# Kernel tuning notes

Hardware: AMD Instinct MI355X
Metric: run time of the kernel (lower is better)

The kernel has to match this reference:

```python
import jax, jax.numpy as jnp
import numpy as np

SR = 22050
L = 2097153            # output_size = int(SR*95.109); equals NFFT//2+1 so spectral broadcast is well-defined
NFFT = 4194304         # 2**ceil(log2(L))
BANDS = [(1.0, 4.0), (4.0, 8.0), (8.0, 13.0), (13.0, 30.0), (30.0, 100.0), (100.0, 200.0)]
SPEC = [7.83, 528.0, 396.0, 2.5, 14.1, 432.0, 6.0, 30.0]
WIN = 15               # min(15, NFFT//100)
FREQS_NP = np.fft.rfftfreq(NFFT, 1.0 / SR).astype(np.float32)
FREQS = jnp.asarray(FREQS_NP)


def _freq_mod(sig, band_w, freq_w, harm_prog, tm_w1, tm_b1, tm_w2, tm_b2, tm_w3, tm_b3):
    t = jnp.arange(L, dtype=jnp.float32)
    Xf = jnp.fft.rfft(jnp.pad(sig, (0, NFFT - L)))            # [L] complex64
    # sequential band enhancements == product of per-band multipliers
    mult = jnp.ones((L,), jnp.float32)
    for b, (lo, hi) in enumerate(BANDS):
        c = (lo + hi) / 2.0
        w = (hi - lo) / 2.0
        mask = jnp.exp(-0.5 * ((FREQS - c) / (w / 2.0)) ** 2)
        mask = jnp.where((FREQS < lo) | (FREQS > hi), 0.0, mask)
        tmod = jnp.sin(2.0 * np.pi * c * t / SR)
        mult = mult * (1.0 + mask * band_w[b] * (1.0 + 0.2 * tmod))
    # harmonic progression (identical for every specific frequency -> compute once)
    tn = (t / L)[:, None]
    h = jax.nn.relu(tn @ tm_w1 + tm_b1)
    h = jax.nn.relu(h @ tm_w2 + tm_b2)
    mp = h @ tm_w3 + tm_b3                                    # [L, 8]
    chord_idx = jnp.floor(t / L * 8.0).astype(jnp.int32) % 8
    chord = harm_prog[chord_idx] * (1.0 + mp[:, 1] * jnp.sin(2.0 * np.pi * t / L))[:, None]
    prog_mean = chord.mean()
    # specific-frequency harmonic windows (static indices; commutative multiplies)
    smult = jnp.ones((L,), jnp.float32)
    for k, f in enumerate(SPEC):
        for m in (1.0, 2.0, 3.0, 4.0, 5.0):
            hf = f * m
            if hf >= SR / 2:
                continue
            hidx = int(np.argmin(np.abs(FREQS_NP - hf)))
            s = max(0, hidx - WIN)
            e = min(L - 1, hidx + WIN)
            win = jnp.asarray(np.exp(-0.5 * ((np.arange(s, e + 1) - hidx) / (WIN / 3.0)) ** 2).astype(np.float32))
            enh = freq_w[k] * win * (1.0 / m ** 1.2) * (1.0 + prog_mean)
            smult = smult.at[s:e + 1].multiply(1.0 + enh)
    Xf = Xf * mult * smult
    mag = jnp.abs(Xf)
    ph = jnp.angle(Xf)
    mag_s = jnp.concatenate([mag[:1], mag[1:-1] * 0.7 + mag[:-2] * 0.15 + mag[2:] * 0.15, mag[-1:]])
    Xc = mag_s * jnp.exp(1j * ph)
    return jnp.fft.irfft(Xc, n=NFFT)[:L]


def _conv1d(x, w, b, stride):
    y = jax.lax.conv_general_dilated(x, w, (stride,), [(2, 2)], dimension_numbers=("NCH", "OIH", "NCH"))
    return y + b[None, :, None]


def setup_inputs() -> dict:
    key = jax.random.key(0)
    ks = jax.random.split(key, 16)
    n = lambda k, s, sc=1.0: jax.random.normal(k, s, dtype=jnp.float32) * sc
    return {
        "z": n(ks[0], (1, 1, L)),
        "condition": n(ks[1], (1, 8)),
        "band_w": jnp.full((6,), 0.5, jnp.float32),
        "freq_w": jnp.full((8,), 0.3, jnp.float32),
        "harm_prog": n(ks[2], (8, 4)),
        "tm_w1": n(ks[3], (1, 32), 0.5), "tm_b1": jnp.zeros((32,), jnp.float32),
        "tm_w2": n(ks[4], (32, 16), 0.2), "tm_b2": jnp.zeros((16,), jnp.float32),
        "tm_w3": n(ks[5], (16, 8), 0.2), "tm_b3": jnp.zeros((8,), jnp.float32),
        "c1_w": n(ks[6], (32, 1, 5), 0.3), "c1_b": jnp.zeros((32,), jnp.float32),
        "c2_w": n(ks[7], (64, 32, 5), 0.08), "c2_b": jnp.zeros((64,), jnp.float32),
        "c3_w": n(ks[8], (128, 64, 5), 0.05), "c3_b": jnp.zeros((128,), jnp.float32),
        "mx_w1": n(ks[9], (192, 256), 0.07), "mx_b1": jnp.zeros((256,), jnp.float32),
        "mx_w2": n(ks[10], (256, 1), 0.06), "mx_b2": jnp.zeros((1,), jnp.float32),
    }


def reference(z, condition, band_w, freq_w, harm_prog, tm_w1, tm_b1, tm_w2, tm_b2, tm_w3, tm_b3,
              c1_w, c1_b, c2_w, c2_b, c3_w, c3_b, mx_w1, mx_b1, mx_w2, mx_b2):
    base = _freq_mod(z[0, 0], band_w, freq_w, harm_prog, tm_w1, tm_b1, tm_w2, tm_b2, tm_w3, tm_b3)[None, None, :]
    h = jax.nn.leaky_relu(_conv1d(base, c1_w, c1_b, 2), 0.2)
    h = jax.nn.leaky_relu(_conv1d(h, c2_w, c2_b, 2), 0.2)
    h = jax.nn.leaky_relu(_conv1d(h, c3_w, c3_b, 2), 0.2)
    feat = h.mean(axis=2)                                     # [1, 128]
    emb = jnp.zeros((1, 64), jnp.float32)                     # instrument_idx=None path
    mixed = jnp.concatenate([feat, emb], axis=1)              # [1, 192]
    out = jax.nn.leaky_relu(mixed @ mx_w1 + mx_b1, 0.2) @ mx_w2 + mx_b2
    return out
```

## Files before the change

### kernel.cpp

```cpp
#include <hip/hip_runtime.h>
#include <cmath>

#define LSIG  2097153
#define MH    2097152
#define NFFTC 4194304
#define NT128 16384
#define O1C   1048577
#define O2C   524289
#define O3C   262145

#define TO3   62
#define NB3   4229

#define A_OFF    0
#define B_OFF    16777216
#define PM_OFF   58720268
#define FEAT_OFF 58720272
#define W2Q_OFF  50331664
#define W3Q_OFF  50352144
#define W1Q_OFF  50434064

struct SmultTab { int hidx[40]; float inv12[40]; int fk[40]; int maxe; };

typedef short short8 __attribute__((ext_vector_type(8)));
typedef float f32x4v __attribute__((ext_vector_type(4)));

union AFrag { uint4 q; short8 s; };
union BFrag { uint4 q; unsigned int u[4]; short8 s; };

__device__ __forceinline__ float lrelu(float a){ return a > 0.0f ? a : 0.2f*a; }

__device__ __forceinline__ float hsin(float rev){ return __builtin_amdgcn_sinf(rev); }
__device__ __forceinline__ float hcos(float rev){ return __builtin_amdgcn_cosf(rev); }

__device__ __forceinline__ unsigned int rbf(float f) {
  unsigned int u = __float_as_uint(f);
  u += 0x7fffu + ((u >> 16) & 1u);
  return u >> 16;
}
__device__ __forceinline__ unsigned int pack_bf2(float a, float b) {
  unsigned int r;
  asm("v_cvt_pk_bf16_f32 %0, %1, %2" : "=v"(r) : "v"(a), "v"(b));
  return r;
}

__device__ __forceinline__ int swz1(int pos, int dw) {
  return (pos*16 + dw) ^ (((pos >> 1) & 7) << 2);
}
__device__ __forceinline__ int swz2(int pos, int dw) {
  return (pos*32 + dw) ^ (((pos >> 1) & 7) << 2);
}

__device__ __forceinline__ int slot128(int jj, int q) {
  int s = q ^ ((q >> 4) & 7);
  return jj*128 + ((s + 9*jj) & 127);
}

__device__ __forceinline__ float2 cadd(float2 a, float2 b){ return make_float2(a.x+b.x, a.y+b.y); }
__device__ __forceinline__ float2 csub(float2 a, float2 b){ return make_float2(a.x-b.x, a.y-b.y); }

template<bool FWD> __device__ __forceinline__ float2 jrot(float2 z){
  return FWD ? make_float2(z.y, -z.x) : make_float2(-z.y, z.x);
}

template<bool FWD> __device__ __forceinline__ void dft8(float2 v[8]) {
  const float cq = 0.70710678118654752440f;
  const float S  = FWD ? -1.0f : 1.0f;
  float2 e0 = cadd(v[0], v[4]), e1 = csub(v[0], v[4]);
  float2 e2 = cadd(v[2], v[6]), e3 = csub(v[2], v[6]);
  float2 E0 = cadd(e0, e2), E2 = csub(e0, e2);
  float2 jt = jrot<FWD>(e3);
  float2 E1 = cadd(e1, jt), E3 = csub(e1, jt);
  float2 o0 = cadd(v[1], v[5]), o1 = csub(v[1], v[5]);
  float2 o2 = cadd(v[3], v[7]), o3 = csub(v[3], v[7]);
  float2 O0 = cadd(o0, o2), O2 = csub(o0, o2);
  float2 jo = jrot<FWD>(o3);
  float2 O1 = cadd(o1, jo), O3 = csub(o1, jo);
  float2 w1 = make_float2(cq*O1.x - S*cq*O1.y, cq*O1.y + S*cq*O1.x);
  float2 w2 = jrot<FWD>(O2);
  float2 w3 = make_float2(-cq*O3.x - S*cq*O3.y, -cq*O3.y + S*cq*O3.x);
  v[0] = cadd(E0, O0); v[4] = csub(E0, O0);
  v[1] = cadd(E1, w1); v[5] = csub(E1, w1);
  v[2] = cadd(E2, w2); v[6] = csub(E2, w2);
  v[3] = cadd(E3, w3); v[7] = csub(E3, w3);
}

template<bool FWD>
__device__ __forceinline__ void fft128_body(float2* stage, int t, int jb, int Ns) {
  const float ssg = FWD ? -1.0f : 1.0f;
  const float invden = 1.0f / (float)(128 * Ns);
  {
    const int jj = t >> 4, b = t & 15;
    const int m = (jb + jj) & (Ns - 1);
    float2 v[8];
#pragma unroll
    for (int a = 0; a < 8; ++a) {
      const int r = 16*a + b;
      float2 x = stage[slot128(jj, r)];
      if (Ns > 1) {
        float rev = (float)(m * r) * invden;
        float sn = ssg * hsin(rev), cs = hcos(rev);
        x = make_float2(x.x*cs - x.y*sn, x.x*sn + x.y*cs);
      }
      v[a] = x;
    }
    dft8<FWD>(v);
#pragma unroll
    for (int d = 0; d < 8; ++d)
      stage[slot128(jj, 16*d + b)] = v[d];
  }
  __syncthreads();
  {
    float2 y[16];
    const int jj = (t & 255) >> 3, d = t & 7;
    if (t < 256) {
#pragma unroll
      for (int b = 0; b < 16; ++b) {
        float2 x = stage[slot128(jj, 16*d + b)];
        float rev = (float)(b*d) * 0.0078125f;
        float sn = ssg * hsin(rev), cs = hcos(rev);
        y[b] = make_float2(x.x*cs - x.y*sn, x.x*sn + x.y*cs);
      }
    }
    __syncthreads();
    if (t < 256) {
      float2 E[8], O[8];
#pragma unroll
      for (int b = 0; b < 8; ++b) { E[b] = y[2*b]; O[b] = y[2*b+1]; }
      dft8<FWD>(E);
      dft8<FWD>(O);
#pragma unroll
      for (int c = 0; c < 8; ++c) {
        float rev = (float)c * 0.0625f;
        float sn = ssg * hsin(rev), cs = hcos(rev);
        float2 To = make_float2(O[c].x*cs - O[c].y*sn, O[c].x*sn + O[c].y*cs);
        stage[slot128(jj, 8*c + d)]      = cadd(E[c], To);
        stage[slot128(jj, 8*c + 64 + d)] = csub(E[c], To);
      }
    }
  }
  __syncthreads();
}

template<bool FWD, bool TRUNC>
__global__ __launch_bounds__(512) void kfft128(const float2* __restrict__ src,
                                               float2* __restrict__ dst, int Ns) {
  __shared__ float2 stage[4096];
  const int t = threadIdx.x;
  const int jb = blockIdx.x * 32;
  for (int c = 0; c < 4; ++c) {
    int u = t + 512*c;
    int jp = u & 15, rr = u >> 4;
    float4 q = *(const float4*)&src[jb + 2*jp + rr*NT128];
    stage[slot128(2*jp,   rr)] = make_float2(q.x, q.y);
    stage[slot128(2*jp+1, rr)] = make_float2(q.z, q.w);
  }
  __syncthreads();
  fft128_body<FWD>(stage, t, jb, Ns);
  if (Ns == 1) {
    for (int c = 0; c < 4; ++c) {
      int u = t + 512*c;
      int jj = u >> 6, k2 = (u & 63) * 2;
      float2 a = stage[slot128(jj, k2)], b = stage[slot128(jj, k2+1)];
      *(float4*)&dst[(jb + jj)*128 + k2] = make_float4(a.x, a.y, b.x, b.y);
    }
  } else {
    for (int c = 0; c < 4; ++c) {
      int u = t + 512*c;
      int pi = u & 15, k = u >> 4;
      int jj = 2*pi, j2 = jb + jj, m2 = j2 & (Ns - 1);
      int base = (j2 - m2)*128 + m2 + k*Ns;
      if (TRUNC && k >= 64) {
        if (k == 64 && j2 == 0) dst[base] = stage[slot128(jj, k)];
        continue;
      }
      float2 a = stage[slot128(jj, k)], b = stage[slot128(jj+1, k)];
      *(float4*)&dst[base] = make_float4(a.x, a.y, b.x, b.y);
    }
  }
}

__global__ __launch_bounds__(512) void kfirst(
    const float* __restrict__ zin, float2* __restrict__ dst,
    const float* __restrict__ tw1, const float* __restrict__ tb1,
    const float* __restrict__ tw2, const float* __restrict__ tb2,
    const float* __restrict__ tw3, const float* __restrict__ tb3,
    const float* __restrict__ hp, float* __restrict__ pm,
    float* __restrict__ feat) {
  __shared__ float2 stage[4096];
  __shared__ float shp[8];
  __shared__ float red[512];
  const int t = threadIdx.x;
  const int bb = blockIdx.x;
  if (bb < 512) {
    const int jb = bb * 32;
    for (int c = 0; c < 4; ++c) {
      int u = t + 512*c;
      int jp = u & 15, rr = u >> 4;
      int n = jb + 2*jp + rr*NT128;
      float2 a0, a1;
      if (n < 1048576) {
        float4 q = *(const float4*)&((const float2*)zin)[n];
        a0 = make_float2(q.x, q.y); a1 = make_float2(q.z, q.w);
      } else if (n == 1048576) {
        a0 = make_float2(zin[2097152], 0.0f); a1 = make_float2(0.0f, 0.0f);
      } else {
        a0 = make_float2(0.0f, 0.0f); a1 = a0;
      }
      stage[slot128(2*jp,   rr)] = a0;
      stage[slot128(2*jp+1, rr)] = a1;
    }
    __syncthreads();
    fft128_body<true>(stage, t, jb, 1);
    for (int c = 0; c < 4; ++c) {
      int u = t + 512*c;
      int jj = u >> 6, k2 = (u & 63) * 2;
      float2 a = stage[slot128(jj, k2)], b = stage[slot128(jj, k2+1)];
      *(float4*)&dst[(jb + jj)*128 + k2] = make_float4(a.x, a.y, b.x, b.y);
    }
    return;
  }
  if (t < 8) { float s = 0.f; for (int j = 0; j < 4; ++j) s += hp[t*4+j]; shp[t] = s; }
  __syncthreads();
  const int gid = (bb - 512)*512 + t;
  if (gid < 32768) feat[gid] = 0.0f;
  const float Lf = 2097153.0f;
  float tnv[4], sv[4];
  int ci[4];
  float acc[4][16];
#pragma unroll
  for (int e = 0; e < 4; ++e) {
    float ti = (float)(gid + e*524288);
    float tn = ti / Lf;
    tnv[e] = tn;
    sv[e] = hsin(tn);
    ci[e] = ((int)floorf(tn * 8.0f)) & 7;
#pragma unroll
    for (int kk = 0; kk < 16; ++kk) acc[e][kk] = tb2[kk];
  }
  for (int j = 0; j < 32; ++j) {
    float a = tw1[j], b = tb1[j];
    float hj[4];
#pragma unroll
    for (int e = 0; e < 4; ++e) hj[e] = fmaxf(a*tnv[e] + b, 0.0f);
#pragma unroll
    for (int kk = 0; kk < 16; ++kk) {
      float w = tw2[j*16 + kk];
#pragma unroll
      for (int e = 0; e < 4; ++e) acc[e][kk] += hj[e]*w;
    }
  }
  float lsum = 0.0f;
  const float b31 = tb3[1];
#pragma unroll
  for (int e = 0; e < 4; ++e) {
    float mp1 = b31;
#pragma unroll
    for (int kk = 0; kk < 16; ++kk) mp1 += fmaxf(acc[e][kk], 0.0f)*tw3[kk*8+1];
    lsum += shp[ci[e]] * (1.0f + mp1*sv[e]);
  }
  if (gid == 0) {
    float ti = 2097152.0f;
    float tn = ti / Lf;
    float a1[16];
    for (int kk = 0; kk < 16; ++kk) a1[kk] = tb2[kk];
    for (int j = 0; j < 32; ++j) {
      float h = fmaxf(tw1[j]*tn + tb1[j], 0.0f);
      for (int kk = 0; kk < 16; ++kk) a1[kk] += h*tw2[j*16+kk];
    }
    float mp1 = b31;
    for (int kk = 0; kk < 16; ++kk) mp1 += fmaxf(a1[kk], 0.0f)*tw3[kk*8+1];
    float svx = hsin(tn);
    int cix = ((int)floorf(tn * 8.0f)) & 7;
    lsum += shp[cix] * (1.0f + mp1*svx);
  }
  red[t] = lsum;
  __syncthreads();
  for (int off = 256; off > 0; off >>= 1) {
    if (t < off) red[t] += red[t+off];
    __syncthreads();
  }
  if (t == 0) atomicAdd(pm, red[0]);
}

__device__ __forceinline__ float2 xsplit(float2 zk, float2 zm, float rev) {
  float2 s  = make_float2(zk.x + zm.x, zk.y - zm.y);
  float2 dd = make_float2(zk.x - zm.x, zk.y + zm.y);
  float sn = -hsin(rev), cs = hcos(rev);
  float2 t1 = make_float2(cs*dd.x - sn*dd.y, cs*dd.y + sn*dd.x);
  return make_float2(0.5f*(s.x + t1.y), 0.5f*(s.y - t1.x));
}
__device__ __forceinline__ float2 scale_xc(float2 c, float mg, float ms) {
  if (mg > 0.0f) { float sc = ms/mg; return make_float2(c.x*sc, c.y*sc); }
  return make_float2(ms, 0.0f);
}
__device__ __forceinline__ float2 invpack(int n, float2 a, float2 b) {
  float2 s  = make_float2(a.x + b.x, a.y - b.y);
  float2 dd = make_float2(a.x - b.x, a.y + b.y);
  float rev = (float)n * (1.0f / (float)NFFTC);
  float sn = hsin(rev), cs = hcos(rev);
  float2 xo = make_float2(0.5f*(cs*dd.x - sn*dd.y), 0.5f*(cs*dd.y + sn*dd.x));
  const float sc = 1.0f / (float)MH;
  return make_float2((0.5f*s.x - xo.y)*sc, (0.5f*s.y + xo.x)*sc);
}

__global__ __launch_bounds__(256) void kspectral(const float2* __restrict__ Z,
    float2* __restrict__ A, const float* __restrict__ bwp,
    const float* __restrict__ fwp, const float* __restrict__ pm_in, SmultTab tab,
    const float* __restrict__ c1w, const float* __restrict__ c2w,
    const float* __restrict__ c3w, unsigned short* __restrict__ w1q,
    unsigned short* __restrict__ w2q, unsigned short* __restrict__ w3q) {
  const int bb = blockIdx.x;
  const int t = threadIdx.x;
  if (bb >= 4096) {
    int i = (bb - 4096)*256 + t;
    if (i < 1024) {
      int e = i & 7, u4 = i >> 3;
      int col = u4 & 15, quad = (u4 >> 4) & 3, mi = u4 >> 6;
      float v = (quad == 0 && e < 5) ? c1w[(mi*16 + col)*5 + e] : 0.0f;
      w1q[i] = (unsigned short)rbf(v);
    }
    if (i < 10240) {
      int e = i & 7, u4 = i >> 3;
      int col = u4 & 15, quad = (u4 >> 4) & 3, mtkt = u4 >> 6;
      int kt = mtkt % 5, mt = mtkt / 5;
      int ch = mt*16 + col, c1 = quad*8 + e;
      w2q[i] = (unsigned short)rbf(c2w[ch*160 + c1*5 + kt]);
    }
    if (i < 40960) {
      int e = i & 7, u4 = i >> 3;
      int col = u4 & 15, quad = (u4 >> 4) & 3, mtkt = u4 >> 6;
      int kt = mtkt % 10, mt = mtkt / 10;
      int ch = mt*16 + col, c2 = (kt & 1)*32 + quad*8 + e;
      w3q[i] = (unsigned short)rbf(c3w[ch*320 + c2*5 + (kt >> 1)]);
    }
    return;
  }
  __shared__ float2 Xlo[258], Xhi[258];
  __shared__ float  Mlo[258], Mhi[258];
  const int k0 = bb * 256;
  const float pm1 = 1.0f + pm_in[0] * (1.0f/8388612.0f);
  for (int w = t; w < 258; w += 256) {
    int k = k0 - 1 + w;
    float2 zk = Z[k & (MH-1)];
    float2 zm = Z[(MH - k) & (MH-1)];
    {
      float2 X = xsplit(zk, zm, (float)k * (1.0f/(float)NFFTC));
      float mv = 1.0f;
      if (k <= 38050) {
        const float blo[6] = {1.0f,4.0f,8.0f,13.0f,30.0f,100.0f};
        const float bhi[6] = {4.0f,8.0f,13.0f,30.0f,100.0f,200.0f};
        const float bcn[6] = {2.5f,6.0f,10.5f,21.5f,65.0f,150.0f};
        const float bhw[6] = {0.75f,1.0f,1.25f,4.25f,17.5f,25.0f};
        float f = (float)((double)k * (22050.0/4194304.0));
#pragma unroll
        for (int b = 0; b < 6; ++b) {
          if (f >= blo[b] && f <= bhi[b]) {
            float q = (f - bcn[b]) / bhw[b];
            float mask = expf(-0.5f*q*q);
            double frd = (double)k * ((double)bcn[b] / 22050.0);
            frd -= floor(frd);
            float tm = hsin((float)frd);
            mv *= (1.0f + mask * bwp[b] * (1.0f + 0.2f*tm));
          }
        }
      }
      if (k <= tab.maxe) {
        for (int ww = 0; ww < 40; ++ww) {
          int dlt = k - tab.hidx[ww];
          if (dlt >= -15 && dlt <= 15) {
            float x = (float)dlt * 0.2f;
            float win = expf(-0.5f*x*x);
            float enh = fwp[tab.fk[ww]] * win * tab.inv12[ww] * pm1;
            mv *= (1.0f + enh);
          }
        }
      }
      X.x *= mv; X.y *= mv;
      Xlo[w] = X; Mlo[w] = sqrtf(X.x*X.x + X.y*X.y);
    }
    {
      float2 X = xsplit(zm, zk, (float)(MH - k) * (1.0f/(float)NFFTC));
      Xhi[w] = X; Mhi[w] = sqrtf(X.x*X.x + X.y*X.y);
    }
  }
  __syncthreads();
  const int k = k0 + t, w = t + 1;
  float msl = (k == 0) ? Mlo[w] : 0.7f*Mlo[w] + 0.15f*(Mlo[w-1] + Mlo[w+1]);
  float2 xl = scale_xc(Xlo[w], Mlo[w], msl);
  float msh = (k == 0) ? Mhi[w] : 0.7f*Mhi[w] + 0.15f*(Mhi[w+1] + Mhi[w-1]);
  float2 xh = scale_xc(Xhi[w], Mhi[w], msh);
  A[k] = invpack(k, xl, xh);
  if (k >= 1) A[MH - k] = invpack(MH - k, xh, xl);
  if (bb == 4095 && t == 255) {
    float2 Xm = Xlo[257]; float Mm = Mlo[257];
    float ms = 0.7f*Mm + 0.15f*(Mlo[256] + Mhi[256]);
    float2 xm = scale_xc(Xm, Mm, ms);
    A[1048576] = invpack(1048576, xm, xm);
  }
}

__global__ __launch_bounds__(256, 4) void kconv(const float* __restrict__ x,
    const unsigned short* __restrict__ w1q, const unsigned short* __restrict__ w2q,
    const unsigned short* __restrict__ w3q, const float* __restrict__ c1b,
    const float* __restrict__ c2b, const float* __restrict__ c3b,
    float* __restrict__ feat) {
  __shared__ float sb[552];
  __shared__ unsigned int sh1[4352];
  __shared__ unsigned int sh2[4224];
  const int tid  = threadIdx.x;
  const int blk  = blockIdx.x;
  const int s3   = blk * TO3;
  const int lane = tid & 63;
  const int wv   = tid >> 6;
  const int col  = lane & 15;
  const int quad = lane >> 4;

  const uint4* W1 = (const uint4*)w1q;
  AFrag a1w[2];
#pragma unroll
  for (int mi = 0; mi < 2; ++mi)
    a1w[mi].q = W1[(mi*4 + quad)*16 + col];

  const uint4* W2 = (const uint4*)w2q;
  const int mt2 = (wv & 1) * 2;
  const int ntb2 = (wv >> 1) * 4;
  uint4 wk2[2][5];
#pragma unroll
  for (int mi = 0; mi < 2; ++mi)
#pragma unroll
    for (int kt = 0; kt < 5; ++kt)
      wk2[mi][kt] = W2[(((mt2+mi)*5 + kt)*4 + quad)*16 + col];

  float b1r[2][4], b2r[2][4];
#pragma unroll
  for (int mi = 0; mi < 2; ++mi)
#pragma unroll
    for (int r = 0; r < 4; ++r) {
      b1r[mi][r] = c1b[mi*16 + quad*4 + r];
      b2r[mi][r] = c2b[(mt2+mi)*16 + quad*4 + r];
    }

  {
    const int pb = 8*s3 - 14;
    for (int idx = tid; idx < 552; idx += 256) {
      int p = pb + idx;
      sb[idx] = (idx < 517 && p >= 0 && p < LSIG) ? x[p] : 0.0f;
    }
    if (tid < 128) sh2[4096 + tid] = 0u;
  }
  __syncthreads();

  {
    const int a1 = 4*s3 - 6;
    for (int nt = wv; nt < 17; nt += 4) {
      const int n = nt*16 + col;
      BFrag bf;
      if (quad == 0) {
        const float* ps = &sb[2*n];
        bf.u[0] = pack_bf2(ps[0], ps[1]);
        bf.u[1] = pack_bf2(ps[2], ps[3]);
        bf.u[2] = pack_bf2(ps[4], ps[5]);
        bf.u[3] = pack_bf2(ps[6], ps[7]);
      } else {
        bf.u[0] = 0u; bf.u[1] = 0u; bf.u[2] = 0u; bf.u[3] = 0u;
      }
      f32x4v acc[2];
      acc[0] = (f32x4v){b1r[0][0], b1r[0][1], b1r[0][2], b1r[0][3]};
      acc[1] = (f32x4v){b1r[1][0], b1r[1][1], b1r[1][2], b1r[1][3]};
      acc[0] = __builtin_amdgcn_mfma_f32_16x16x32_bf16(a1w[0].s, bf.s, acc[0], 0, 0, 0);
      acc[1] = __builtin_amdgcn_mfma_f32_16x16x32_bf16(a1w[1].s, bf.s, acc[1], 0, 0, 0);
      const int o1 = a1 + n;
      const bool ok = (n <= 257) && (o1 >= 0) && (o1 < O1C);
#pragma unroll
      for (int mi = 0; mi < 2; ++mi) {
        float v0 = ok ? lrelu(acc[mi][0]) : 0.0f;
        float v1 = ok ? lrelu(acc[mi][1]) : 0.0f;
        float v2 = ok ? lrelu(acc[mi][2]) : 0.0f;
        float v3 = ok ? lrelu(acc[mi][3]) : 0.0f;
        uint2 pk; pk.x = pack_bf2(v0, v1); pk.y = pack_bf2(v2, v3);
        *(uint2*)&sh1[swz1(n, mi*8 + quad*2)] = pk;
      }
    }
  }
  __syncthreads();

  f32x4v acc2[2][4];
#pragma unroll
  for (int mi = 0; mi < 2; ++mi)
#pragma unroll
    for (int nt = 0; nt < 4; ++nt)
      acc2[mi][nt] = (f32x4v){b2r[mi][0], b2r[mi][1], b2r[mi][2], b2r[mi][3]};
#pragma unroll
  for (int kt = 0; kt < 5; ++kt) {
#pragma unroll
    for (int nt = 0; nt < 4; ++nt) {
      const int n = (ntb2 + nt)*16 + col;
      const int row = 2*n + kt;
      BFrag bf;
      bf.q = *(const uint4*)&sh1[swz1(row, quad*4)];
      AFrag a0, a1; a0.q = wk2[0][kt]; a1.q = wk2[1][kt];
      acc2[0][nt] = __builtin_amdgcn_mfma_f32_16x16x32_bf16(a0.s, bf.s, acc2[0][nt], 0, 0, 0);
      acc2[1][nt] = __builtin_amdgcn_mfma_f32_16x16x32_bf16(a1.s, bf.s, acc2[1][nt], 0, 0, 0);
    }
  }

  {
    const int a2 = 2*s3 - 2;
#pragma unroll
    for (int nt = 0; nt < 4; ++nt) {
      const int p = (ntb2 + nt)*16 + col;
      const int o2 = a2 + p;
      const bool ok = (o2 >= 0) && (o2 < O2C);
#pragma unroll
      for (int mi = 0; mi < 2; ++mi) {
        float v0 = ok ? lrelu(acc2[mi][nt][0]) : 0.0f;
        float v1 = ok ? lrelu(acc2[mi][nt][1]) : 0.0f;
        float v2 = ok ? lrelu(acc2[mi][nt][2]) : 0.0f;
        float v3 = ok ? lrelu(acc2[mi][nt][3]) : 0.0f;
        const int dwb = (mt2+mi)*8 + quad*2;
        uint2 pk; pk.x = pack_bf2(v0, v1); pk.y = pack_bf2(v2, v3);
        *(uint2*)&sh2[swz2(p, dwb)] = pk;
      }
    }
  }
  __syncthreads();

  {
    const uint4* W3 = (const uint4*)w3q;
    const int slot = (blk & 255) * 128;
#pragma unroll
    for (int pass = 0; pass < 2; ++pass) {
      const int mt = wv + 4*pass;
      uint4 wk3[10];
#pragma unroll
      for (int kt = 0; kt < 10; ++kt)
        wk3[kt] = W3[((mt*10 + kt)*4 + quad)*16 + col];
      float b3r[4];
#pragma unroll
      for (int r = 0; r < 4; ++r) b3r[r] = c3b[mt*16 + quad*4 + r];
      f32x4v acc3[4];
#pragma unroll
      for (int nt = 0; nt < 4; ++nt)
        acc3[nt] = (f32x4v){b3r[0], b3r[1], b3r[2], b3r[3]};
#pragma unroll
      for (int kt = 0; kt < 10; ++kt) {
        const int tap = kt >> 1;
        const int hh  = (kt & 1) * 16;
#pragma unroll
        for (int nt = 0; nt < 4; ++nt) {
          const int n = nt*16 + col;
          const int row = 2*n + tap;
          BFrag bf;
          bf.q = *(const uint4*)&sh2[swz2(row, hh + quad*4)];
          AFrag a; a.q = wk3[kt];
          acc3[nt] = __builtin_amdgcn_mfma_f32_16x16x32_bf16(a.s, bf.s, acc3[nt], 0, 0, 0);
        }
      }
#pragma unroll
      for (int r = 0; r < 4; ++r) {
        const int ch = mt*16 + quad*4 + r;
        float v = 0.0f;
#pragma unroll
        for (int nt = 0; nt < 4; ++nt) {
          const int n = nt*16 + col;
          const bool ok = (n < TO3) && (s3 + n < O3C);
          if (ok) v += lrelu(acc3[nt][r]);
        }
        v += __shfl_xor(v, 1);
        v += __shfl_xor(v, 2);
        v += __shfl_xor(v, 4);
        v += __shfl_xor(v, 8);
        if (col == 0) atomicAdd(&feat[slot + ch], v);
      }
    }
  }
}

__global__ __launch_bounds__(256) void kfinal(const float* __restrict__ feat,
    const float* __restrict__ mw1, const float* __restrict__ mb1,
    const float* __restrict__ mw2, const float* __restrict__ mb2,
    float* __restrict__ out) {
  __shared__ float sfeat[128];
  __shared__ float red[256];
  const int tid = threadIdx.x;
  if (tid < 128) {
    float s = 0.0f;
    for (int sl = 0; sl < 256; ++sl) s += feat[sl*128 + tid];
    sfeat[tid] = s / 262145.0f;
  }
  __syncthreads();
  float y = mb1[tid];
  for (int i = 0; i < 128; ++i) y += sfeat[i] * mw1[i*256 + tid];
  y = y > 0.0f ? y : 0.2f*y;
  red[tid] = y * mw2[tid];
  __syncthreads();
  for (int off = 128; off > 0; off >>= 1) {
    if (tid < off) red[tid] += red[tid+off];
    __syncthreads();
  }
  if (tid == 0) out[0] = red[0] + mb2[0];
}

extern "C" void kernel_launch(void* const* d_in, const int* in_sizes, int n_in,
                              void* d_out, int out_size, void* d_ws, size_t ws_size,
                              hipStream_t stream) {
  (void)in_sizes; (void)n_in; (void)out_size; (void)ws_size;
  const float* z   = (const float*)d_in[0];
  const float* bw  = (const float*)d_in[2];
  const float* fw  = (const float*)d_in[3];
  const float* hp  = (const float*)d_in[4];
  const float* tw1 = (const float*)d_in[5];
  const float* tb1 = (const float*)d_in[6];
  const float* tw2 = (const float*)d_in[7];
  const float* tb2 = (const float*)d_in[8];
  const float* tw3 = (const float*)d_in[9];
  const float* tb3 = (const float*)d_in[10];
  const float* c1w = (const float*)d_in[11];
  const float* c1b = (const float*)d_in[12];
  const float* c2w = (const float*)d_in[13];
  const float* c2b = (const float*)d_in[14];
  const float* c3w = (const float*)d_in[15];
  const float* c3b = (const float*)d_in[16];
  const float* mw1 = (const float*)d_in[17];
  const float* mb1 = (const float*)d_in[18];
  const float* mw2 = (const float*)d_in[19];
  const float* mb2 = (const float*)d_in[20];

  char* wsb = (char*)d_ws;
  float2* A    = (float2*)(wsb + A_OFF);
  float2* B    = (float2*)(wsb + B_OFF);
  float*  PM   = (float*)(wsb + PM_OFF);
  float*  FEAT = (float*)(wsb + FEAT_OFF);
  unsigned short* W1Q = (unsigned short*)(wsb + W1Q_OFF);
  unsigned short* W2Q = (unsigned short*)(wsb + W2Q_OFF);
  unsigned short* W3Q = (unsigned short*)(wsb + W3Q_OFF);

  SmultTab tab;
  {
    const double spec[8] = {7.83, 528.0, 396.0, 2.5, 14.1, 432.0, 6.0, 30.0};
    int n = 0, maxe = 0;
    for (int kk = 0; kk < 8; ++kk)
      for (int m = 1; m <= 5; ++m) {
        double hf = spec[kk] * (double)m;
        if (hf >= 11025.0) continue;
        int hidx = (int)std::floor(hf * (4194304.0/22050.0) + 0.5);
        tab.hidx[n]  = hidx;
        tab.inv12[n] = (float)(1.0/std::pow((double)m, 1.2));
        tab.fk[n]    = kk;
        if (hidx + 15 > maxe) maxe = hidx + 15;
        ++n;
      }
    tab.maxe = maxe;
  }

  (void)hipMemsetAsync(wsb + PM_OFF, 0, 4, stream);

  kfirst<<<1536,512,0,stream>>>(z, A, tw1,tb1,tw2,tb2,tw3,tb3,hp, PM, FEAT);

  kfft128<true,false><<<512,512,0,stream>>>(A, B, 128);
  kfft128<true,false><<<512,512,0,stream>>>(B, A, 16384);

  kspectral<<<4256,256,0,stream>>>(A, B, bw, fw, PM, tab, c1w, c2w, c3w, W1Q, W2Q, W3Q);

  kfft128<false,false><<<512,512,0,stream>>>(B, A, 1);
  kfft128<false,false><<<512,512,0,stream>>>(A, B, 128);
  kfft128<false,true ><<<512,512,0,stream>>>(B, A, 16384);

  kconv<<<NB3,256,0,stream>>>((const float*)A, W1Q, W2Q, W3Q, c1b, c2b, c3b, FEAT);
  kfinal<<<1,256,0,stream>>>(FEAT, mw1, mb1, mw2, mb2, (float*)d_out);
}
```

Before: 254.7 us.

## Double conv tile per block and use all FFT threads in final radix-16 stage

```diff
diff --git a/kernel.cpp b/kernel.cpp
--- a/kernel.cpp
+++ b/kernel.cpp
@@ -9,8 +9,8 @@
 #define O2C   524289
 #define O3C   262145
 
-#define TO3   62
-#define NB3   4229
+#define TO3   124
+#define NB3   2115
 
 #define A_OFF    0
 #define B_OFF    16777216
@@ -111,32 +111,33 @@
   }
   __syncthreads();
   {
-    float2 y[16];
-    const int jj = (t & 255) >> 3, d = t & 7;
-    if (t < 256) {
-#pragma unroll
-      for (int b = 0; b < 16; ++b) {
-        float2 x = stage[slot128(jj, 16*d + b)];
-        float rev = (float)(b*d) * 0.0078125f;
-        float sn = ssg * hsin(rev), cs = hcos(rev);
-        y[b] = make_float2(x.x*cs - x.y*sn, x.x*sn + x.y*cs);
-      }
-    }
-    __syncthreads();
-    if (t < 256) {
-      float2 E[8], O[8];
-#pragma unroll
-      for (int b = 0; b < 8; ++b) { E[b] = y[2*b]; O[b] = y[2*b+1]; }
-      dft8<FWD>(E);
-      dft8<FWD>(O);
+    const int jj = t >> 4, d = (t >> 1) & 7, par = t & 1;
+    float2 h[8];
+#pragma unroll
+    for (int bp = 0; bp < 8; ++bp) {
+      const int b = 2*bp + par;
+      float2 x = stage[slot128(jj, 16*d + b)];
+      float rev = (float)(b*d) * 0.0078125f;
+      float sn = ssg * hsin(rev), cs = hcos(rev);
+      h[bp] = make_float2(x.x*cs - x.y*sn, x.x*sn + x.y*cs);
+    }
+    dft8<FWD>(h);
+    if (par) {
 #pragma unroll
       for (int c = 0; c < 8; ++c) {
         float rev = (float)c * 0.0625f;
         float sn = ssg * hsin(rev), cs = hcos(rev);
-        float2 To = make_float2(O[c].x*cs - O[c].y*sn, O[c].x*sn + O[c].y*cs);
-        stage[slot128(jj, 8*c + d)]      = cadd(E[c], To);
-        stage[slot128(jj, 8*c + 64 + d)] = csub(E[c], To);
-      }
+        h[c] = make_float2(h[c].x*cs - h[c].y*sn, h[c].x*sn + h[c].y*cs);
+      }
+    }
+    __syncthreads();
+    const float sgn = par ? -1.0f : 1.0f;
+    const int off = d + (par << 6);
+#pragma unroll
+    for (int c = 0; c < 8; ++c) {
+      float px = __shfl_xor(h[c].x, 1);
+      float py = __shfl_xor(h[c].y, 1);
+      stage[slot128(jj, 8*c + off)] = make_float2(px + sgn*h[c].x, py + sgn*h[c].y);
     }
   }
   __syncthreads();
@@ -400,14 +401,14 @@
   }
 }
 
-__global__ __launch_bounds__(256, 4) void kconv(const float* __restrict__ x,
+__global__ __launch_bounds__(512, 4) void kconv(const float* __restrict__ x,
     const unsigned short* __restrict__ w1q, const unsigned short* __restrict__ w2q,
     const unsigned short* __restrict__ w3q, const float* __restrict__ c1b,
     const float* __restrict__ c2b, const float* __restrict__ c3b,
     float* __restrict__ feat) {
-  __shared__ float sb[552];
-  __shared__ unsigned int sh1[4352];
-  __shared__ unsigned int sh2[4224];
+  __shared__ float sb[1064];
+  __shared__ unsigned int sh1[8448];
+  __shared__ unsigned int sh2[8448];
   const int tid  = threadIdx.x;
   const int blk  = blockIdx.x;
   const int s3   = blk * TO3;
@@ -443,17 +444,17 @@
 
   {
     const int pb = 8*s3 - 14;
-    for (int idx = tid; idx < 552; idx += 256) {
+    for (int idx = tid; idx < 1064; idx += 512) {
       int p = pb + idx;
-      sb[idx] = (idx < 517 && p >= 0 && p < LSIG) ? x[p] : 0.0f;
-    }
-    if (tid < 128) sh2[4096 + tid] = 0u;
+      sb[idx] = (idx < 1005 && p >= 0 && p < LSIG) ? x[p] : 0.0f;
+    }
+    if (tid < 256) sh2[8192 + tid] = 0u;
   }
   __syncthreads();
 
   {
     const int a1 = 4*s3 - 6;
-    for (int nt = wv; nt < 17; nt += 4) {
+    for (int nt = wv; nt < 33; nt += 8) {
       const int n = nt*16 + col;
       BFrag bf;
       if (quad == 0) {
@@ -471,7 +472,7 @@
       acc[0] = __builtin_amdgcn_mfma_f32_16x16x32_bf16(a1w[0].s, bf.s, acc[0], 0, 0, 0);
       acc[1] = __builtin_amdgcn_mfma_f32_16x16x32_bf16(a1w[1].s, bf.s, acc[1], 0, 0, 0);
       const int o1 = a1 + n;
-      const bool ok = (n <= 257) && (o1 >= 0) && (o1 < O1C);
+      const bool ok = (n <= 507) && (o1 >= 0) && (o1 < O1C);
 #pragma unroll
       for (int mi = 0; mi < 2; ++mi) {
         float v0 = ok ? lrelu(acc[mi][0]) : 0.0f;
@@ -529,50 +530,47 @@
   {
     const uint4* W3 = (const uint4*)w3q;
     const int slot = (blk & 255) * 128;
-#pragma unroll
-    for (int pass = 0; pass < 2; ++pass) {
-      const int mt = wv + 4*pass;
-      uint4 wk3[10];
-#pragma unroll
-      for (int kt = 0; kt < 10; ++kt)
-        wk3[kt] = W3[((mt*10 + kt)*4 + quad)*16 + col];
-      float b3r[4];
-#pragma unroll
-      for (int r = 0; r < 4; ++r) b3r[r] = c3b[mt*16 + quad*4 + r];
-      f32x4v acc3[4];
-#pragma unroll
-      for (int nt = 0; nt < 4; ++nt)
-        acc3[nt] = (f32x4v){b3r[0], b3r[1], b3r[2], b3r[3]};
-#pragma unroll
-      for (int kt = 0; kt < 10; ++kt) {
-        const int tap = kt >> 1;
-        const int hh  = (kt & 1) * 16;
-#pragma unroll
-        for (int nt = 0; nt < 4; ++nt) {
-          const int n = nt*16 + col;
-          const int row = 2*n + tap;
-          BFrag bf;
-          bf.q = *(const uint4*)&sh2[swz2(row, hh + quad*4)];
-          AFrag a; a.q = wk3[kt];
-          acc3[nt] = __builtin_amdgcn_mfma_f32_16x16x32_bf16(a.s, bf.s, acc3[nt], 0, 0, 0);
-        }
-      }
-#pragma unroll
-      for (int r = 0; r < 4; ++r) {
-        const int ch = mt*16 + quad*4 + r;
-        float v = 0.0f;
-#pragma unroll
-        for (int nt = 0; nt < 4; ++nt) {
-          const int n = nt*16 + col;
-          const bool ok = (n < TO3) && (s3 + n < O3C);
-          if (ok) v += lrelu(acc3[nt][r]);
-        }
-        v += __shfl_xor(v, 1);
-        v += __shfl_xor(v, 2);
-        v += __shfl_xor(v, 4);
-        v += __shfl_xor(v, 8);
-        if (col == 0) atomicAdd(&feat[slot + ch], v);
-      }
+    const int mt = wv;
+    uint4 wk3[10];
+#pragma unroll
+    for (int kt = 0; kt < 10; ++kt)
+      wk3[kt] = W3[((mt*10 + kt)*4 + quad)*16 + col];
+    float b3r[4];
+#pragma unroll
+    for (int r = 0; r < 4; ++r) b3r[r] = c3b[mt*16 + quad*4 + r];
+    f32x4v acc3[8];
+#pragma unroll
+    for (int nt = 0; nt < 8; ++nt)
+      acc3[nt] = (f32x4v){b3r[0], b3r[1], b3r[2], b3r[3]};
+#pragma unroll
+    for (int kt = 0; kt < 10; ++kt) {
+      const int tap = kt >> 1;
+      const int hh  = (kt & 1) * 16;
+#pragma unroll
+      for (int nt = 0; nt < 8; ++nt) {
+        const int n = nt*16 + col;
+        const int row = 2*n + tap;
+        BFrag bf;
+        bf.q = *(const uint4*)&sh2[swz2(row, hh + quad*4)];
+        AFrag a; a.q = wk3[kt];
+        acc3[nt] = __builtin_amdgcn_mfma_f32_16x16x32_bf16(a.s, bf.s, acc3[nt], 0, 0, 0);
+      }
+    }
+#pragma unroll
+    for (int r = 0; r < 4; ++r) {
+      const int ch = mt*16 + quad*4 + r;
+      float v = 0.0f;
+#pragma unroll
+      for (int nt = 0; nt < 8; ++nt) {
+        const int n = nt*16 + col;
+        const bool ok = (n < TO3) && (s3 + n < O3C);
+        if (ok) v += lrelu(acc3[nt][r]);
+      }
+      v += __shfl_xor(v, 1);
+      v += __shfl_xor(v, 2);
+      v += __shfl_xor(v, 4);
+      v += __shfl_xor(v, 8);
+      if (col == 0) atomicAdd(&feat[slot + ch], v);
     }
   }
 }
@@ -667,6 +665,6 @@
   kfft128<false,false><<<512,512,0,stream>>>(A, B, 128);
   kfft128<false,true ><<<512,512,0,stream>>>(B, A, 16384);
 
-  kconv<<<NB3,256,0,stream>>>((const float*)A, W1Q, W2Q, W3Q, c1b, c2b, c3b, FEAT);
+  kconv<<<NB3,512,0,stream>>>((const float*)A, W1Q, W2Q, W3Q, c1b, c2b, c3b, FEAT);
   kfinal<<<1,256,0,stream>>>(FEAT, mw1, mb1, mw2, mb2, (float*)d_out);
 }
```

Result: no change. 259.5 us (+1.9%).
